# Kernel optimization log

Hardware: AMD Instinct MI355X
Metric: run time of the kernel (lower is better)

Reference implementation:

```python
import jax, jax.numpy as jnp
import numpy as np
from math import pi

N_TRAJS, N_RES, N_BINS = 20, 300, 34
DIST_BIN_CENTRES = jnp.asarray(np.array([3.75 + 0.5 * i for i in range(N_BINS)], dtype=np.float32))
SIG = 1.25            # gauss_sigma
K_CB_DIST = 150.0
K_HB_DIST = 5.0
K_HB_GEN = 0.0
K_ANG_HB_GEN = 0.0
W_VIOL_MIN = 3.0      # weight_violate_min
EXP_MIN = 1.0         # pairwise_exponent_min
EXP_MAX = 0.75        # pairwise_exponent_max
HB_CUTOFF = 6.0       # hb_cutoff_gen
CUTOFF = 40.0         # pairwise_force_cutoff


def _norm(d):
    # safe euclidean norm over last axis (avoids NaN grad at exactly 0)
    return jnp.sqrt(jnp.maximum((d * d).sum(axis=-1), 1e-12))


def _safe_pow(x, p):
    pos = x > 0
    return jnp.where(pos, jnp.where(pos, x, 1.0) ** p, 0.0)


def _angle_forces(ba, bc, k, close, true_ang):
    ba_n = _norm(ba)
    bc_n = _norm(bc)
    cosang = jnp.clip((ba * bc).sum(-1) / jnp.clip(ba_n * bc_n, 0.1, 100.0), -1.0 + 1e-6, 1.0 - 1e-6)
    forces = k * close * (jnp.arccos(cosang) - true_ang)
    cr = jnp.cross(ba, bc)
    fa_vec = jnp.cross(-ba, cr)
    fc_vec = jnp.cross(bc, cr)
    fa = forces[..., None] * fa_vec / jnp.maximum(_norm(fa_vec), 0.1)[..., None]
    fc = forces[..., None] * fc_vec / jnp.maximum(_norm(fc_vec), 0.1)[..., None]
    fb = -fa - fc
    return fa, fb, fc


def setup_inputs() -> dict:
    key = jax.random.key(0)
    ks = jax.random.split(key, 9)
    B, R = N_TRAJS, N_RES
    base = jax.random.uniform(ks[0], (B, R, 3), dtype=jnp.float32) * 30.0
    def off(k):
        return base + jax.random.normal(k, (B, R, 3), dtype=jnp.float32)
    coords_N = off(ks[1]); coords_C = off(ks[2]); coords_O = off(ks[3])
    coords_CB = off(ks[4]); coords_H = off(ks[5])
    gaussian_weights = jax.random.normal(ks[6], (R, R, N_BINS), dtype=jnp.float32)
    hb_dists_min = 1.5 + 1.5 * jax.random.uniform(ks[7], (R, R), dtype=jnp.float32)
    hb_dists_max = hb_dists_min + 1.0 + 2.0 * jax.random.uniform(ks[8], (R, R), dtype=jnp.float32)
    return {"coords_N": coords_N, "coords_C": coords_C, "coords_O": coords_O,
            "coords_CB": coords_CB, "coords_H": coords_H,
            "gaussian_weights": gaussian_weights,
            "hb_dists_min": hb_dists_min, "hb_dists_max": hb_dists_max}


def reference(coords_N, coords_C, coords_O, coords_CB, coords_H,
              gaussian_weights, hb_dists_min, hb_dists_max):
    B, R, _ = coords_CB.shape
    idx = jnp.arange(R)
    # mask excluding |i-j| <= 2 (self and near-diagonal), as in the torch diag_mask
    diag_mask = (jnp.abs(idx[:, None] - idx[None, :]) > 2).astype(jnp.float32)[None]

    # --- CB distogram gaussian pairwise forces ---
    diffs_cb = coords_CB[:, None, :, :] - coords_CB[:, :, None, :]   # [B,i,j,3] = cb_j - cb_i
    dists_cb = jnp.clip(_norm(diffs_cb), 0.1, CUTOFF)                 # [B,i,j]
    norm_cb = diffs_cb / dists_cb[..., None]
    dfm = dists_cb[..., None] - DIST_BIN_CENTRES                      # [B,i,j,K]
    cb_e = gaussian_weights[None] * jnp.exp(-0.5 * (dfm / SIG) ** 2) / SIG
    f_cb = (-dfm / (SIG * SIG) * cb_e).sum(axis=3)                    # [B,i,j]
    pair_cb = -f_cb[..., None] * K_CB_DIST * norm_cb
    accs_CB = pair_cb.sum(axis=1)

    # --- H..O hydrogen-bond min/max distance restraints ---
    diffs_ho = coords_O[:, None, :, :] - coords_H[:, :, None, :]      # [B,i,j,3] = o_j - h_i
    dists_ho = jnp.clip(_norm(diffs_ho), 0.1, CUTOFF)
    norm_ho = diffs_ho / dists_ho[..., None]
    v_min = jnp.maximum(hb_dists_min[None] - dists_ho, 0.0)
    v_max = jnp.maximum(dists_ho - hb_dists_max[None], 0.0)
    close = (dists_ho < HB_CUTOFF).astype(jnp.float32) * diag_mask
    v_max_gen = close * jnp.maximum(dists_ho - HB_CUTOFF, 0.0)
    f_min = W_VIOL_MIN * K_HB_DIST * _safe_pow(v_min, EXP_MIN)
    f_max = K_HB_DIST * _safe_pow(v_max, EXP_MAX) + K_HB_GEN * _safe_pow(v_max_gen, EXP_MAX)
    pair_hb = (f_min - f_max)[..., None] * norm_ho
    accs_H = -pair_hb.sum(axis=2)
    accs_O = pair_hb.sum(axis=1)

    # --- O-H-N angle term (k_ang_hb_gen = 0, kept for fidelity) ---
    diffs_hn = (coords_N - coords_H)[:, :, None, :]                   # [B,i,1,3], broadcast over j
    fa, fb, fc = _angle_forces(diffs_ho, diffs_hn, K_ANG_HB_GEN, close, pi)
    accs_O = accs_O + fa.sum(axis=1)
    accs_H = accs_H + fb.sum(axis=2)
    accs_N = fc.sum(axis=2)

    # --- C-O-H angle term ---
    diffs_oc = (coords_C - coords_O)[:, :, None, :]                   # [B,i,1,3]
    fa2, fb2, fc2 = _angle_forces(diffs_oc, -diffs_ho, K_ANG_HB_GEN, close, pi)
    accs_C = fa2.sum(axis=2)
    accs_O = accs_O + fb2.sum(axis=1)
    accs_H = accs_H + fc2.sum(axis=2)

    return (accs_N, accs_C, accs_O, accs_CB, accs_H)
```

## Files before the change

kernel.cpp:

```cpp
#include <hip/hip_runtime.h>

#define NRES  300
#define NTRJ  20
#define NBINS 34
#define PLANE (NTRJ * NRES * 3)
#define IC    2
#define NCH   150
#define NCBB  (5 * NCH)
#define NHCH  15
#define NHBB  (5 * NHCH)
#define OFF_H (2 * NCH)
#define NPLANES (2 * NCH + NHCH)
#define WROWP 36
#define NRED  ((PLANE + 255) / 256)

#define EXP2F(x) __builtin_exp2f(x)
#define LOG2F(x) __builtin_log2f(x)

template <bool PART>
__global__ __launch_bounds__(256)
void force_fused(const float* __restrict__ cO, const float* __restrict__ cCB,
                 const float* __restrict__ cH, const float* __restrict__ gw,
                 const float* __restrict__ hmin, const float* __restrict__ hmax,
                 float* __restrict__ out, float* __restrict__ part) {
  __shared__ __align__(16) float smem[3800];

  const int tid  = threadIdx.x;
  const int wv   = tid >> 6;
  const int lane = tid & 63;

  if (blockIdx.x < NCBB) {
    float* wbufw = smem + wv * (16 * WROWP);
    float* sIC   = smem + 4 * (16 * WROWP);

    const int bsub = lane >> 4;
    const int jsub = lane & 15;
    const int jt   = blockIdx.x % 5;
    const int ch   = blockIdx.x / 5;
    const int i0   = ch * IC;
    const int j0w  = jt * 64 + wv * 16;
    const int j    = j0w + jsub;
    const bool jv  = (j < NRES);
    const int jc   = jv ? j : NRES - 1;
    const int E2   = 17 * min(16, max(0, NRES - j0w));

    for (int e = tid; e < NTRJ * IC * 6; e += 256) {
      const int b = e / (IC * 6), r = e % (IC * 6);
      const int ii = r / 6, c = r % 6;
      const int comp = (c < 3) ? c : c - 3;
      const int src = ((b * NRES) + i0 + ii) * 3 + comp;
      sIC[(b * IC + ii) * 8 + (c < 3 ? c : c + 1)] = (c < 3) ? cCB[src] : cH[src];
    }
    __syncthreads();

    float pjx[5], pjy[5], pjz[5], pox[5], poy[5], poz[5];
    float acx[5] = {}, acy[5] = {}, acz[5] = {};
    float aox[5] = {}, aoy[5] = {}, aoz[5] = {};
#pragma unroll
    for (int q = 0; q < 5; ++q) {
      const int b = bsub * 5 + q;
      const float* p = cCB + ((size_t)(b * NRES + jc)) * 3;
      pjx[q] = p[0]; pjy[q] = p[1]; pjz[q] = p[2];
      const float* o = cO + ((size_t)(b * NRES + jc)) * 3;
      pox[q] = o[0]; poy[q] = o[1]; poz[q] = o[2];
    }

    float2 r2[5];
    {
      const float2* src = (const float2*)gw + ((size_t)i0 * NRES + j0w) * 17;
#pragma unroll
      for (int u = 0; u < 5; ++u) {
        const int e = lane + u * 64;
        r2[u] = (e < E2) ? src[e] : make_float2(0.f, 0.f);
      }
    }

    for (int ii = 0; ii < IC; ++ii) {
      const int i = i0 + ii;
#pragma unroll
      for (int u = 0; u < 5; ++u) {
        const int e = lane + u * 64;
        if (e < 272) {
          const int row = e / 17, col = e - row * 17;
          ((float2*)wbufw)[row * 18 + col] = r2[u];
        }
      }
      if (ii + 1 < IC) {
        const float2* src =
            (const float2*)gw + ((size_t)(i + 1) * NRES + j0w) * 17;
#pragma unroll
        for (int u = 0; u < 5; ++u) {
          const int e = lane + u * 64;
          r2[u] = (e < E2) ? src[e] : make_float2(0.f, 0.f);
        }
      }

      float w[36];
      {
        const float4* wp = (const float4*)&wbufw[jsub * WROWP];
#pragma unroll
        for (int k4 = 0; k4 < 9; ++k4) {
          float4 v = wp[k4];
          w[4*k4+0] = v.x; w[4*k4+1] = v.y; w[4*k4+2] = v.z; w[4*k4+3] = v.w;
        }
        w[34] = 0.f; w[35] = 0.f;
      }

      const float hmn = hmin[i * NRES + jc];
      const float hmx = hmax[i * NRES + jc];

#pragma unroll
      for (int q = 0; q < 5; ++q) {
        const int b = bsub * 5 + q;
        const float4* ic4 = (const float4*)&sIC[(b * IC + ii) * 8];
        const float4 cb = ic4[0];
        const float4 hh = ic4[1];

        float dx = pjx[q] - cb.x, dy = pjy[q] - cb.y, dz = pjz[q] - cb.z;
        float d2 = fmaf(dx, dx, fmaf(dy, dy, dz * dz));
        d2 = fminf(fmaxf(d2, 0.01f), 1600.0f);
        float rinv = __frsqrt_rn(d2);
        float d    = d2 * rinv;
        float dA = d - 3.75f, dB = d - 9.75f, dC = d - 15.75f;
        float gA = EXP2F(-0.46166241f * dA * dA);
        float mA = EXP2F(fmaf(0.46166241f, dA, -0.11541560f));
        float gB = EXP2F(-0.46166241f * dB * dB);
        float mB = EXP2F(fmaf(0.46166241f, dB, -0.11541560f));
        float gC = EXP2F(-0.46166241f * dC * dC);
        float mC = EXP2F(fmaf(0.46166241f, dC, -0.11541560f));
        float s0 = 0.f, s1 = 0.f, s2 = 0.f;
#pragma unroll
        for (int k = 0; k < 12; ++k) {
          s0 = fmaf(w[k]      * dA, gA, s0); gA *= mA; mA *= 0.85214379f; dA -= 0.5f;
          s1 = fmaf(w[k + 12] * dB, gB, s1); gB *= mB; mB *= 0.85214379f; dB -= 0.5f;
          s2 = fmaf(w[k + 24] * dC, gC, s2); gC *= mC; mC *= 0.85214379f; dC -= 0.5f;
        }
        float cf = 76.8f * ((s0 + s1) + s2) * rinv;
        acx[q] = fmaf(cf, dx, acx[q]);
        acy[q] = fmaf(cf, dy, acy[q]);
        acz[q] = fmaf(cf, dz, acz[q]);

        float ex = pox[q] - hh.x, ey = poy[q] - hh.y, ez = poz[q] - hh.z;
        float e2 = fmaf(ex, ex, fmaf(ey, ey, ez * ez));
        e2 = fminf(fmaxf(e2, 0.01f), 1600.0f);
        float rh = __frsqrt_rn(e2);
        float dh = e2 * rh;
        float vmin = fmaxf(hmn - dh, 0.0f);
        float vmax = fmaxf(dh - hmx, 0.0f);
        float fmn = 15.0f * vmin;
        float fmx = (vmax > 0.0f) ? 5.0f * EXP2F(0.75f * LOG2F(vmax)) : 0.0f;
        float ff = (fmn - fmx) * rh;
        aox[q] = fmaf(ff, ex, aox[q]);
        aoy[q] = fmaf(ff, ey, aoy[q]);
        aoz[q] = fmaf(ff, ez, aoz[q]);
      }
    }

    if (jv) {
      if constexpr (PART) {
        float* pc  = part + (size_t)ch * PLANE;
        float* po2 = part + (size_t)(NCH + ch) * PLANE;
#pragma unroll
        for (int q = 0; q < 5; ++q) {
          const int base = ((bsub * 5 + q) * NRES + j) * 3;
          pc[base + 0]  = acx[q]; pc[base + 1]  = acy[q]; pc[base + 2]  = acz[q];
          po2[base + 0] = aox[q]; po2[base + 1] = aoy[q]; po2[base + 2] = aoz[q];
        }
      } else {
#pragma unroll
        for (int q = 0; q < 5; ++q) {
          const int base = ((bsub * 5 + q) * NRES + j) * 3;
          atomicAdd(&out[3 * PLANE + base + 0], acx[q]);
          atomicAdd(&out[3 * PLANE + base + 1], acy[q]);
          atomicAdd(&out[3 * PLANE + base + 2], acz[q]);
          atomicAdd(&out[2 * PLANE + base + 0], aox[q]);
          atomicAdd(&out[2 * PLANE + base + 1], aoy[q]);
          atomicAdd(&out[2 * PLANE + base + 2], aoz[q]);
        }
      }
    }
  } else {
    float* tmn = smem;
    float* tmx = smem + 1300;
    float* sO  = smem + 2600;

    const int bx2 = blockIdx.x - NCBB;
    const int it  = bx2 % 5;
    const int jch = bx2 / 5;
    const int j0  = jch * 20;
    const int i   = it * 64 + lane;
    const bool iv = (i < NRES);
    const int icl = iv ? i : NRES - 1;
    const int b0  = __builtin_amdgcn_readfirstlane(wv) * 5;

    for (int e = tid; e < 64 * 20; e += 256) {
      const int row = e / 20, col = e - (e / 20) * 20;
      int ig = it * 64 + row; if (ig > NRES - 1) ig = NRES - 1;
      tmn[col * 65 + row] = hmin[ig * NRES + j0 + col];
      tmx[col * 65 + row] = hmax[ig * NRES + j0 + col];
    }
    for (int e = tid; e < NTRJ * 20 * 3; e += 256) {
      const int b = e / 60, r = e % 60;
      sO[e] = cO[((b * NRES) + j0 + r / 3) * 3 + (r % 3)];
    }

    float phx[5], phy[5], phz[5];
    float ahx[5] = {}, ahy[5] = {}, ahz[5] = {};
#pragma unroll
    for (int q = 0; q < 5; ++q) {
      const float* h = cH + ((size_t)((b0 + q) * NRES + icl)) * 3;
      phx[q] = h[0]; phy[q] = h[1]; phz[q] = h[2];
    }
    __syncthreads();

    for (int jj = 0; jj < 20; ++jj) {
      const float hmn = tmn[jj * 65 + lane];
      const float hmx = tmx[jj * 65 + lane];
#pragma unroll
      for (int q = 0; q < 5; ++q) {
        const float* po = &sO[((b0 + q) * 20 + jj) * 3];
        float ex = po[0] - phx[q], ey = po[1] - phy[q], ez = po[2] - phz[q];
        float e2 = fmaf(ex, ex, fmaf(ey, ey, ez * ez));
        e2 = fminf(fmaxf(e2, 0.01f), 1600.0f);
        float rh = __frsqrt_rn(e2);
        float dh = e2 * rh;
        float vmin = fmaxf(hmn - dh, 0.0f);
        float vmax = fmaxf(dh - hmx, 0.0f);
        float fmn = 15.0f * vmin;
        float fmx = (vmax > 0.0f) ? 5.0f * EXP2F(0.75f * LOG2F(vmax)) : 0.0f;
        float ff = (fmn - fmx) * rh;
        ahx[q] = fmaf(-ff, ex, ahx[q]);
        ahy[q] = fmaf(-ff, ey, ahy[q]);
        ahz[q] = fmaf(-ff, ez, ahz[q]);
      }
    }
    if (iv) {
      if constexpr (PART) {
        float* hp = part + (size_t)(OFF_H + jch) * PLANE;
#pragma unroll
        for (int q = 0; q < 5; ++q) {
          const int base = ((b0 + q) * NRES + i) * 3;
          hp[base + 0] = ahx[q]; hp[base + 1] = ahy[q]; hp[base + 2] = ahz[q];
        }
      } else {
#pragma unroll
        for (int q = 0; q < 5; ++q) {
          const int base = ((b0 + q) * NRES + i) * 3;
          atomicAdd(&out[4 * PLANE + base + 0], ahx[q]);
          atomicAdd(&out[4 * PLANE + base + 1], ahy[q]);
          atomicAdd(&out[4 * PLANE + base + 2], ahz[q]);
        }
      }
    }
  }
}

__global__ __launch_bounds__(256)
void reduce_seg(const float* __restrict__ part, float* __restrict__ out) {
  const int seg  = blockIdx.x / NRED;
  const int t    = (blockIdx.x % NRED) * 256 + threadIdx.x;
  if (t >= PLANE) return;

  int c0, cnt;
  if (seg < 3)      { c0 = seg * 50;             cnt = 50; }
  else if (seg < 6) { c0 = NCH + (seg - 3) * 50; cnt = 50; }
  else              { c0 = OFF_H;                cnt = NHCH; }

  const float* p = part + t + (size_t)c0 * PLANE;
  float s[5] = {};
  for (int c = 0; c < cnt; c += 5) {
#pragma unroll
    for (int u = 0; u < 5; ++u) s[u] += p[(size_t)(c + u) * PLANE];
  }
  const float tot = ((s[0] + s[1]) + (s[2] + s[3])) + s[4];
  if (seg < 3)      atomicAdd(&out[3 * PLANE + t], tot);
  else if (seg < 6) atomicAdd(&out[2 * PLANE + t], tot);
  else              out[4 * PLANE + t] = tot;
}

extern "C" void kernel_launch(void* const* d_in, const int* in_sizes, int n_in,
                              void* d_out, int out_size, void* d_ws, size_t ws_size,
                              hipStream_t stream) {
  const float* cO  = (const float*)d_in[2];
  const float* cCB = (const float*)d_in[3];
  const float* cH  = (const float*)d_in[4];
  const float* gw  = (const float*)d_in[5];
  const float* hmn = (const float*)d_in[6];
  const float* hmx = (const float*)d_in[7];
  float* out  = (float*)d_out;
  float* part = (float*)d_ws;

  (void)hipMemsetAsync(out, 0, (size_t)out_size * sizeof(float), stream);

  if (ws_size >= (size_t)NPLANES * PLANE * sizeof(float)) {
    force_fused<true><<<dim3(NCBB + NHBB), dim3(256), 0, stream>>>(
        cO, cCB, cH, gw, hmn, hmx, out, part);
    reduce_seg<<<dim3(7 * NRED), dim3(256), 0, stream>>>(part, out);
  } else {
    force_fused<false><<<dim3(NCBB + NHBB), dim3(256), 0, stream>>>(
        cO, cCB, cH, gw, hmn, hmx, out, nullptr);
  }
}
```

Before: 41.54 us.

## Split HB-O force into dedicated blocks and drop memset via direct reduce writes

The CB-pair blocks no longer compute the H-bond force on O. That work moves to 75 new blocks that tile over 20 i-rows each, which shrinks the O partial planes from 150 to 15. The reduction kernel now writes results directly instead of using atomics, and it zeroes the N and C outputs itself. This removes the memset and cuts partial-plane traffic in the partial path. The cost is an extra block class and somewhat more divergent kernel code.

```diff
diff --git a/kernel.cpp b/kernel.cpp
--- a/kernel.cpp
+++ b/kernel.cpp
@@ -7,11 +7,11 @@
 #define IC    2
 #define NCH   150
 #define NCBB  (5 * NCH)
-#define NHCH  15
-#define NHBB  (5 * NHCH)
-#define OFF_H (2 * NCH)
-#define NPLANES (2 * NCH + NHCH)
-#define WROWP 36
+#define NOB   75
+#define NHB   75
+#define OFF_O 150
+#define OFF_H 165
+#define NPL   180
 #define NRED  ((PLANE + 255) / 256)
 
 #define EXP2F(x) __builtin_exp2f(x)
@@ -30,8 +30,8 @@
   const int lane = tid & 63;
 
   if (blockIdx.x < NCBB) {
-    float* wbufw = smem + wv * (16 * WROWP);
-    float* sIC   = smem + 4 * (16 * WROWP);
+    float* wbufw = smem + wv * (16 * 36);
+    float* sIC   = smem + 4 * (16 * 36);
 
     const int bsub = lane >> 4;
     const int jsub = lane & 15;
@@ -44,25 +44,18 @@
     const int jc   = jv ? j : NRES - 1;
     const int E2   = 17 * min(16, max(0, NRES - j0w));
 
-    for (int e = tid; e < NTRJ * IC * 6; e += 256) {
-      const int b = e / (IC * 6), r = e % (IC * 6);
-      const int ii = r / 6, c = r % 6;
-      const int comp = (c < 3) ? c : c - 3;
-      const int src = ((b * NRES) + i0 + ii) * 3 + comp;
-      sIC[(b * IC + ii) * 8 + (c < 3 ? c : c + 1)] = (c < 3) ? cCB[src] : cH[src];
+    for (int e = tid; e < NTRJ * IC * 3; e += 256) {
+      const int b = e / (IC * 3), r = e % (IC * 3);
+      sIC[(b * IC + r / 3) * 4 + (r % 3)] = cCB[((b * NRES) + i0 + r / 3) * 3 + (r % 3)];
     }
     __syncthreads();
 
-    float pjx[5], pjy[5], pjz[5], pox[5], poy[5], poz[5];
+    float pjx[5], pjy[5], pjz[5];
     float acx[5] = {}, acy[5] = {}, acz[5] = {};
-    float aox[5] = {}, aoy[5] = {}, aoz[5] = {};
 #pragma unroll
     for (int q = 0; q < 5; ++q) {
-      const int b = bsub * 5 + q;
-      const float* p = cCB + ((size_t)(b * NRES + jc)) * 3;
+      const float* p = cCB + ((size_t)((bsub * 5 + q) * NRES + jc)) * 3;
       pjx[q] = p[0]; pjy[q] = p[1]; pjz[q] = p[2];
-      const float* o = cO + ((size_t)(b * NRES + jc)) * 3;
-      pox[q] = o[0]; poy[q] = o[1]; poz[q] = o[2];
     }
 
     float2 r2[5];
@@ -76,7 +69,6 @@
     }
 
     for (int ii = 0; ii < IC; ++ii) {
-      const int i = i0 + ii;
 #pragma unroll
       for (int u = 0; u < 5; ++u) {
         const int e = lane + u * 64;
@@ -87,7 +79,7 @@
       }
       if (ii + 1 < IC) {
         const float2* src =
-            (const float2*)gw + ((size_t)(i + 1) * NRES + j0w) * 17;
+            (const float2*)gw + ((size_t)(i0 + ii + 1) * NRES + j0w) * 17;
 #pragma unroll
         for (int u = 0; u < 5; ++u) {
           const int e = lane + u * 64;
@@ -97,7 +89,7 @@
 
       float w[36];
       {
-        const float4* wp = (const float4*)&wbufw[jsub * WROWP];
+        const float4* wp = (const float4*)&wbufw[jsub * 36];
 #pragma unroll
         for (int k4 = 0; k4 < 9; ++k4) {
           float4 v = wp[k4];
@@ -106,16 +98,9 @@
         w[34] = 0.f; w[35] = 0.f;
       }
 
-      const float hmn = hmin[i * NRES + jc];
-      const float hmx = hmax[i * NRES + jc];
-
 #pragma unroll
       for (int q = 0; q < 5; ++q) {
-        const int b = bsub * 5 + q;
-        const float4* ic4 = (const float4*)&sIC[(b * IC + ii) * 8];
-        const float4 cb = ic4[0];
-        const float4 hh = ic4[1];
-
+        const float4 cb = *(const float4*)&sIC[((bsub * 5 + q) * IC + ii) * 4];
         float dx = pjx[q] - cb.x, dy = pjy[q] - cb.y, dz = pjz[q] - cb.z;
         float d2 = fmaf(dx, dx, fmaf(dy, dy, dz * dz));
         d2 = fminf(fmaxf(d2, 0.01f), 1600.0f);
@@ -139,8 +124,59 @@
         acx[q] = fmaf(cf, dx, acx[q]);
         acy[q] = fmaf(cf, dy, acy[q]);
         acz[q] = fmaf(cf, dz, acz[q]);
-
-        float ex = pox[q] - hh.x, ey = poy[q] - hh.y, ez = poz[q] - hh.z;
+      }
+    }
+
+    if (jv) {
+      if constexpr (PART) {
+        float* pc = part + (size_t)ch * PLANE;
+#pragma unroll
+        for (int q = 0; q < 5; ++q) {
+          const int base = ((bsub * 5 + q) * NRES + j) * 3;
+          pc[base + 0] = acx[q]; pc[base + 1] = acy[q]; pc[base + 2] = acz[q];
+        }
+      } else {
+#pragma unroll
+        for (int q = 0; q < 5; ++q) {
+          const int base = ((bsub * 5 + q) * NRES + j) * 3;
+          atomicAdd(&out[3 * PLANE + base + 0], acx[q]);
+          atomicAdd(&out[3 * PLANE + base + 1], acy[q]);
+          atomicAdd(&out[3 * PLANE + base + 2], acz[q]);
+        }
+      }
+    }
+  } else if (blockIdx.x < NCBB + NOB) {
+    float* sH = smem;
+    const int bx2 = blockIdx.x - NCBB;
+    const int jt  = bx2 % 5;
+    const int ich = bx2 / 5;
+    const int i0  = ich * 20;
+    const int j   = jt * 64 + lane;
+    const bool jv = (j < NRES);
+    const int jc  = jv ? j : NRES - 1;
+    const int b0  = wv * 5;
+
+    for (int e = tid; e < NTRJ * 20 * 3; e += 256) {
+      const int b = e / 60, r = e % 60;
+      sH[e] = cH[((b * NRES) + i0 + r / 3) * 3 + (r % 3)];
+    }
+    float pox[5], poy[5], poz[5];
+    float aox[5] = {}, aoy[5] = {}, aoz[5] = {};
+#pragma unroll
+    for (int q = 0; q < 5; ++q) {
+      const float* o = cO + ((size_t)((b0 + q) * NRES + jc)) * 3;
+      pox[q] = o[0]; poy[q] = o[1]; poz[q] = o[2];
+    }
+    __syncthreads();
+
+    for (int ii = 0; ii < 20; ++ii) {
+      const int i = i0 + ii;
+      const float hmn = hmin[i * NRES + jc];
+      const float hmx = hmax[i * NRES + jc];
+#pragma unroll
+      for (int q = 0; q < 5; ++q) {
+        const float* ph = &sH[((b0 + q) * 20 + ii) * 3];
+        float ex = pox[q] - ph[0], ey = poy[q] - ph[1], ez = poz[q] - ph[2];
         float e2 = fmaf(ex, ex, fmaf(ey, ey, ez * ez));
         e2 = fminf(fmaxf(e2, 0.01f), 1600.0f);
         float rh = __frsqrt_rn(e2);
@@ -155,24 +191,18 @@
         aoz[q] = fmaf(ff, ez, aoz[q]);
       }
     }
-
     if (jv) {
       if constexpr (PART) {
-        float* pc  = part + (size_t)ch * PLANE;
-        float* po2 = part + (size_t)(NCH + ch) * PLANE;
-#pragma unroll
-        for (int q = 0; q < 5; ++q) {
-          const int base = ((bsub * 5 + q) * NRES + j) * 3;
-          pc[base + 0]  = acx[q]; pc[base + 1]  = acy[q]; pc[base + 2]  = acz[q];
+        float* po2 = part + (size_t)(OFF_O + ich) * PLANE;
+#pragma unroll
+        for (int q = 0; q < 5; ++q) {
+          const int base = ((b0 + q) * NRES + j) * 3;
           po2[base + 0] = aox[q]; po2[base + 1] = aoy[q]; po2[base + 2] = aoz[q];
         }
       } else {
 #pragma unroll
         for (int q = 0; q < 5; ++q) {
-          const int base = ((bsub * 5 + q) * NRES + j) * 3;
-          atomicAdd(&out[3 * PLANE + base + 0], acx[q]);
-          atomicAdd(&out[3 * PLANE + base + 1], acy[q]);
-          atomicAdd(&out[3 * PLANE + base + 2], acz[q]);
+          const int base = ((b0 + q) * NRES + j) * 3;
           atomicAdd(&out[2 * PLANE + base + 0], aox[q]);
           atomicAdd(&out[2 * PLANE + base + 1], aoy[q]);
           atomicAdd(&out[2 * PLANE + base + 2], aoz[q]);
@@ -183,15 +213,14 @@
     float* tmn = smem;
     float* tmx = smem + 1300;
     float* sO  = smem + 2600;
-
-    const int bx2 = blockIdx.x - NCBB;
-    const int it  = bx2 % 5;
-    const int jch = bx2 / 5;
+    const int bx3 = blockIdx.x - NCBB - NOB;
+    const int it  = bx3 % 5;
+    const int jch = bx3 / 5;
     const int j0  = jch * 20;
     const int i   = it * 64 + lane;
     const bool iv = (i < NRES);
     const int icl = iv ? i : NRES - 1;
-    const int b0  = __builtin_amdgcn_readfirstlane(wv) * 5;
+    const int b0  = wv * 5;
 
     for (int e = tid; e < 64 * 20; e += 256) {
       const int row = e / 20, col = e - (e / 20) * 20;
@@ -203,7 +232,6 @@
       const int b = e / 60, r = e % 60;
       sO[e] = cO[((b * NRES) + j0 + r / 3) * 3 + (r % 3)];
     }
-
     float phx[5], phy[5], phz[5];
     float ahx[5] = {}, ahy[5] = {}, ahz[5] = {};
 #pragma unroll
@@ -257,25 +285,31 @@
 
 __global__ __launch_bounds__(256)
 void reduce_seg(const float* __restrict__ part, float* __restrict__ out) {
-  const int seg  = blockIdx.x / NRED;
-  const int t    = (blockIdx.x % NRED) * 256 + threadIdx.x;
+  const int seg = blockIdx.x / NRED;
+  const int t   = (blockIdx.x % NRED) * 256 + threadIdx.x;
   if (t >= PLANE) return;
 
-  int c0, cnt;
-  if (seg < 3)      { c0 = seg * 50;             cnt = 50; }
-  else if (seg < 6) { c0 = NCH + (seg - 3) * 50; cnt = 50; }
-  else              { c0 = OFF_H;                cnt = NHCH; }
-
-  const float* p = part + t + (size_t)c0 * PLANE;
-  float s[5] = {};
-  for (int c = 0; c < cnt; c += 5) {
-#pragma unroll
-    for (int u = 0; u < 5; ++u) s[u] += p[(size_t)(c + u) * PLANE];
+  if (seg == 0) {
+    const float* p = part + t;
+    float s[6] = {};
+    for (int c = 0; c < 150; c += 6) {
+#pragma unroll
+      for (int u = 0; u < 6; ++u) s[u] += p[(size_t)(c + u) * PLANE];
+    }
+    out[3 * PLANE + t] = ((s[0] + s[1]) + (s[2] + s[3])) + (s[4] + s[5]);
+  } else {
+    const int c0 = (seg == 1) ? OFF_O : OFF_H;
+    const float* p = part + t + (size_t)c0 * PLANE;
+    float s[5] = {};
+#pragma unroll
+    for (int c = 0; c < 15; c += 5) {
+#pragma unroll
+      for (int u = 0; u < 5; ++u) s[u] += p[(size_t)(c + u) * PLANE];
+    }
+    const float tot = ((s[0] + s[1]) + (s[2] + s[3])) + s[4];
+    if (seg == 1) { out[2 * PLANE + t] = tot; out[0 * PLANE + t] = 0.f; }
+    else          { out[4 * PLANE + t] = tot; out[1 * PLANE + t] = 0.f; }
   }
-  const float tot = ((s[0] + s[1]) + (s[2] + s[3])) + s[4];
-  if (seg < 3)      atomicAdd(&out[3 * PLANE + t], tot);
-  else if (seg < 6) atomicAdd(&out[2 * PLANE + t], tot);
-  else              out[4 * PLANE + t] = tot;
 }
 
 extern "C" void kernel_launch(void* const* d_in, const int* in_sizes, int n_in,
@@ -290,14 +324,13 @@
   float* out  = (float*)d_out;
   float* part = (float*)d_ws;
 
-  (void)hipMemsetAsync(out, 0, (size_t)out_size * sizeof(float), stream);
-
-  if (ws_size >= (size_t)NPLANES * PLANE * sizeof(float)) {
-    force_fused<true><<<dim3(NCBB + NHBB), dim3(256), 0, stream>>>(
+  if (ws_size >= (size_t)NPL * PLANE * sizeof(float)) {
+    force_fused<true><<<dim3(NCBB + NOB + NHB), dim3(256), 0, stream>>>(
         cO, cCB, cH, gw, hmn, hmx, out, part);
-    reduce_seg<<<dim3(7 * NRED), dim3(256), 0, stream>>>(part, out);
+    reduce_seg<<<dim3(3 * NRED), dim3(256), 0, stream>>>(part, out);
   } else {
-    force_fused<false><<<dim3(NCBB + NHBB), dim3(256), 0, stream>>>(
+    (void)hipMemsetAsync(out, 0, (size_t)out_size * sizeof(float), stream);
+    force_fused<false><<<dim3(NCBB + NOB + NHB), dim3(256), 0, stream>>>(
         cO, cCB, cH, gw, hmn, hmx, out, nullptr);
   }
 }
```

Result: slower. 50.62 us (+21.9%).
